# Kernel tuning notes

Measured on AMD Instinct MI355X. Metric: run time of the kernel, lower is better.

## Reference

```python
import jax, jax.numpy as jnp
import numpy as np

NUM_POINTS = 16384
OVERSAMPLE = 3
IMPORTANCE_RATIO = 0.75


def point_sample(feat, coords):
    """grid_sample(bilinear, align_corners=False, zero padding) at [0,1]^2 coords.
    feat: (N, C, H, W); coords: (N, P, 2) with coords[...,0]=x (width), [...,1]=y.
    Returns (N, C, P)."""
    N, C, H, W = feat.shape
    # grid_sample with g = 2c-1, align_corners=False -> pixel = c*size - 0.5
    x = coords[..., 0] * W - 0.5
    y = coords[..., 1] * H - 0.5
    x0 = jnp.floor(x)
    y0 = jnp.floor(y)
    x1 = x0 + 1.0
    y1 = y0 + 1.0
    wx1 = x - x0
    wx0 = 1.0 - wx1
    wy1 = y - y0
    wy0 = 1.0 - wy1
    featf = feat.reshape(N, C, H * W)

    def gather(yi, xi):
        valid = (xi >= 0) & (xi <= W - 1) & (yi >= 0) & (yi <= H - 1)
        xic = jnp.clip(xi, 0, W - 1).astype(jnp.int32)
        yic = jnp.clip(yi, 0, H - 1).astype(jnp.int32)
        idx = yic * W + xic  # (N, P)
        v = jnp.take_along_axis(featf, idx[:, None, :], axis=2)  # (N, C, P)
        return v * valid[:, None, :].astype(feat.dtype)

    out = (gather(y0, x0) * (wy0 * wx0)[:, None, :]
           + gather(y0, x1) * (wy0 * wx1)[:, None, :]
           + gather(y1, x0) * (wy1 * wx0)[:, None, :]
           + gather(y1, x1) * (wy1 * wx1)[:, None, :])
    return out


def calculate_uncertainty(logits):
    """logits: (N, C, P) -> (N, P) uncertainty = top2 - top1 (<= 0)."""
    if logits.shape[1] == 1:
        return -jnp.abs(logits)[:, 0, :]
    top2 = jax.lax.top_k(jnp.moveaxis(logits, 1, -1), 2)[0]  # (N, P, 2)
    return top2[..., 1] - top2[..., 0]


def sample_point_coords(coarse_logits):
    """get_uncertain_point_coords_with_randomness (torch.no_grad branch)."""
    N = coarse_logits.shape[0]
    num_sampled = NUM_POINTS * OVERSAMPLE
    num_imp = int(IMPORTANCE_RATIO * NUM_POINTS)
    num_rand = NUM_POINTS - num_imp
    k1, k2 = jax.random.split(jax.random.key(7))
    cand = jax.random.uniform(k1, (N, num_sampled, 2), dtype=jnp.float32)
    cand_logits = point_sample(coarse_logits, cand)  # (N, C, S)
    unc = calculate_uncertainty(cand_logits)  # (N, S)
    idx = jax.lax.top_k(unc, num_imp)[1]  # (N, num_imp)
    imp = jnp.take_along_axis(cand, idx[..., None], axis=1)  # (N, num_imp, 2)
    rand = jax.random.uniform(k2, (N, num_rand, 2), dtype=jnp.float32)
    return jnp.concatenate([imp, rand], axis=1)  # (N, P, 2)


def point_head(fine, coarse_pts, w0, b0, w1, b1, w2, b2, wp, bp):
    x = jnp.concatenate([fine, coarse_pts], axis=1)  # (N, nin+C, P)
    for w, b in ((w0, b0), (w1, b1), (w2, b2)):
        x = jax.nn.relu(jnp.einsum('oc,ncp->nop', w, x) + b[None, :, None])
        x = jnp.concatenate([x, coarse_pts], axis=1)  # coarse_pred_each_layer
    return jnp.einsum('oc,ncp->nop', wp, x) + bp[None, :, None]  # (N, C, P)


def setup_inputs() -> dict:
    key = jax.random.key(0)
    ks = jax.random.split(key, 8)
    N, C, Hc, Wc = 8, 19, 64, 64
    nin, Hf, Wf = 256, 128, 128
    fin = nin + C  # 275
    return {
        'coarse_sem_seg_logits': jax.random.normal(ks[0], (N, C, Hc, Wc), jnp.float32),
        'features': jax.random.normal(ks[1], (N, nin, Hf, Wf), jnp.float32),
        'w0': jax.random.normal(ks[2], (nin, fin), jnp.float32) * (2.0 / fin) ** 0.5,
        'b0': jnp.zeros((nin,), jnp.float32),
        'w1': jax.random.normal(ks[3], (nin, fin), jnp.float32) * (2.0 / fin) ** 0.5,
        'b1': jnp.zeros((nin,), jnp.float32),
        'w2': jax.random.normal(ks[4], (nin, fin), jnp.float32) * (2.0 / fin) ** 0.5,
        'b2': jnp.zeros((nin,), jnp.float32),
        'wp': jax.random.normal(ks[5], (C, fin), jnp.float32) * 0.001,
        'bp': jnp.zeros((C,), jnp.float32),
    }


def reference(coarse_sem_seg_logits, features, w0, b0, w1, b1, w2, b2, wp, bp):
    # training-mode forward of PointRendSemSegHead
    point_coords = jax.lax.stop_gradient(
        sample_point_coords(jax.lax.stop_gradient(coarse_sem_seg_logits)))
    coarse_pts = point_sample(coarse_sem_seg_logits, point_coords)  # (N, C, P)
    fine_pts = point_sample(features, point_coords)  # (N, nin, P)
    point_logits = point_head(fine_pts, coarse_pts, w0, b0, w1, b1, w2, b2, wp, bp)
    return coarse_sem_seg_logits, point_logits, point_coords
```

## Files before the change

### kernel.cpp

```cpp
#include <hip/hip_runtime.h>
#include <stdint.h>

#pragma clang fp contract(off)

#define NB    8
#define CCH   19
#define CSTR  20
#define FCH   256
#define FIN   275
#define KP    288
#define NPTS  16384
#define NSAMP 49152
#define NIMP  12288
#define NRAND 4096
#define SORT_M 65536
#define CHUNK  8192
#define TP    64
#define XROW  608
#define WBF_OFF (4u << 20)
#define CTR_OFF (4718592u)
#define FTR_OFF (8u << 20)
#define FTR_BYTES (134217728ull / 2)

typedef __attribute__((ext_vector_type(8))) short bf16x8;
typedef __attribute__((ext_vector_type(4))) float f32x4;

__host__ __device__ __forceinline__ uint32_t rotl32(uint32_t v, int r) {
  return (v << r) | (v >> (32 - r));
}

__host__ __device__ __forceinline__ void tf2x32(uint32_t k0, uint32_t k1,
                                                uint32_t x0, uint32_t x1,
                                                uint32_t* o0, uint32_t* o1) {
  const uint32_t ks2 = k0 ^ k1 ^ 0x1BD11BDAu;
  x0 += k0; x1 += k1;
#define TF_R(r) { x0 += x1; x1 = rotl32(x1, (r)); x1 ^= x0; }
  TF_R(13) TF_R(15) TF_R(26) TF_R(6)
  x0 += k1;  x1 += ks2 + 1u;
  TF_R(17) TF_R(29) TF_R(16) TF_R(24)
  x0 += ks2; x1 += k0 + 2u;
  TF_R(13) TF_R(15) TF_R(26) TF_R(6)
  x0 += k0;  x1 += k1 + 3u;
  TF_R(17) TF_R(29) TF_R(16) TF_R(24)
  x0 += k1;  x1 += ks2 + 4u;
  TF_R(13) TF_R(15) TF_R(26) TF_R(6)
  x0 += ks2; x1 += k0 + 5u;
#undef TF_R
  *o0 = x0; *o1 = x1;
}

__device__ __forceinline__ float u01_at(uint32_t k0, uint32_t k1, uint32_t i) {
  uint32_t o0, o1;
  tf2x32(k0, k1, 0u, i, &o0, &o1);
  const uint32_t b = o0 ^ o1;
  const float f = __uint_as_float((b >> 9) | 0x3f800000u) - 1.0f;
  return fmaxf(0.0f, f);
}

__device__ __forceinline__ unsigned short f2bf(float f) {
  const uint32_t u = __float_as_uint(f);
  return (unsigned short)((u + 0x7fffu + ((u >> 16) & 1u)) >> 16);
}

__device__ __forceinline__ float bf2f(unsigned short h) {
  return __uint_as_float((uint32_t)h << 16);
}

template <int SZ>
__device__ __forceinline__ void interp(float cx, float cy, int* off, float* wgt) {
  const float X = cx * (float)SZ - 0.5f, Y = cy * (float)SZ - 0.5f;
  const float x0f = floorf(X), y0f = floorf(Y);
  const float fx = X - x0f, fy = Y - y0f;
  const float wx0 = 1.0f - fx, wy0 = 1.0f - fy;
  const int x0 = (int)x0f, y0 = (int)y0f;
  const int x0c = min(max(x0, 0), SZ - 1), x1c = min(max(x0 + 1, 0), SZ - 1);
  const int y0c = min(max(y0, 0), SZ - 1), y1c = min(max(y0 + 1, 0), SZ - 1);
  const bool vx0 = (x0 >= 0) & (x0 <= SZ - 1), vx1 = (x0 >= -1) & (x0 <= SZ - 2);
  const bool vy0 = (y0 >= 0) & (y0 <= SZ - 1), vy1 = (y0 >= -1) & (y0 <= SZ - 2);
  off[0] = y0c * SZ + x0c; wgt[0] = (vy0 & vx0) ? wy0 * wx0 : 0.0f;
  off[1] = y0c * SZ + x1c; wgt[1] = (vy0 & vx1) ? wy0 * fx  : 0.0f;
  off[2] = y1c * SZ + x0c; wgt[2] = (vy1 & vx0) ? fy  * wx0 : 0.0f;
  off[3] = y1c * SZ + x1c; wgt[3] = (vy1 & vx1) ? fy  * fx  : 0.0f;
}

__device__ __forceinline__ void ftr_tile_load(const float* __restrict__ feats,
                                              int ti, int tt,
                                              unsigned short (*tile)[66]) {
  const int nn = ti >> 10, ct = (ti >> 8) & 3, pt = ti & 255;
  const int c0 = ct * 64, p0 = pt * 64;
  const float* src = feats + ((size_t)nn << 22);
#pragma unroll 4
  for (int k = 0; k < 16; ++k) {
    const int c = 4 * k + (tt >> 6);
    const int p = tt & 63;
    tile[p][c] = f2bf(src[((size_t)(c0 + c) << 14) + p0 + p]);
  }
}

__device__ __forceinline__ void ftr_tile_store(unsigned short* __restrict__ ftr,
                                               int ti, int tt,
                                               unsigned short (*tile)[66]) {
  const int nn = ti >> 10, ct = (ti >> 8) & 3, pt = ti & 255;
  const int c0 = ct * 64, p0 = pt * 64;
  const int p = tt >> 2, q = tt & 3;
  const int cb = q * 16;
  uint32_t w[8];
#pragma unroll
  for (int m = 0; m < 8; ++m)
    w[m] = (uint32_t)tile[p][cb + 2 * m] | ((uint32_t)tile[p][cb + 2 * m + 1] << 16);
  unsigned short* dst = ftr + ((((size_t)nn << 14) + p0 + p) << 8) + c0 + cb;
  *(uint4*)(dst)     = make_uint4(w[0], w[1], w[2], w[3]);
  *(uint4*)(dst + 8) = make_uint4(w[4], w[5], w[6], w[7]);
}

__global__ __launch_bounds__(256) void prep(
    const float* __restrict__ coarse, float* __restrict__ ctr,
    const float* __restrict__ w0, const float* __restrict__ w1,
    const float* __restrict__ w2, const float* __restrict__ wpw,
    unsigned short* __restrict__ wbf, unsigned short* __restrict__ wpb) {
  __shared__ float tile[CCH][257];
  const int b = blockIdx.x, t = threadIdx.x;
  if (b < 128) {
    const int nn = b >> 4, px0 = (b & 15) * 256;
    const float* src = coarse + (size_t)nn * (CCH * 4096) + px0;
#pragma unroll
    for (int c = 0; c < CCH; ++c) tile[c][t] = src[c * 4096 + t];
    __syncthreads();
    float v[CSTR];
#pragma unroll
    for (int c = 0; c < CCH; ++c) v[c] = tile[c][t];
    v[19] = 0.0f;
    float* dst = ctr + ((size_t)(nn << 12) + px0 + t) * CSTR;
#pragma unroll
    for (int k = 0; k < 5; ++k) {
      f32x4 x; x[0] = v[4*k]; x[1] = v[4*k+1]; x[2] = v[4*k+2]; x[3] = v[4*k+3];
      *(f32x4*)(dst + 4 * k) = x;
    }
  } else {
    const int i = (b - 128) * 256 + t;
    if (i < 3 * 256 * KP) {
      const int L = i / (256 * KP);
      const int rem = i - L * (256 * KP);
      const int o = rem / KP, k = rem - o * KP;
      const float* W = (L == 0) ? w0 : (L == 1) ? w1 : w2;
      wbf[i] = (k < FIN) ? f2bf(W[o * FIN + k]) : (unsigned short)0;
    } else {
      const int j = i - 3 * 256 * KP;
      const int o = j / KP, k = j - o * KP;
      wpb[j] = (o < CCH && k < FIN) ? f2bf(wpw[o * FIN + k]) : (unsigned short)0;
    }
  }
}

__global__ __launch_bounds__(256) void unc_tr(
    const float* __restrict__ ctr, unsigned long long* __restrict__ keys,
    const float* __restrict__ feats, unsigned short* __restrict__ ftr,
    uint32_t k1a, uint32_t k1b, int tile0, int use_tr) {
  __shared__ unsigned short tile[64][66];
  const int bid = blockIdx.x, t = threadIdx.x;
  if (bid < 2048) {
    const int tid = bid * 256 + t;
    const int nn = tid >> 16, s = tid & (SORT_M - 1);
    if (s >= NSAMP) { keys[tid] = 0xFFFFFFFFFFFFFFFFull; return; }
    const uint32_t ci = (uint32_t)(((unsigned)nn * NSAMP + (unsigned)s) * 2);
    const float cx = u01_at(k1a, k1b, ci);
    const float cy = u01_at(k1a, k1b, ci + 1);
    const float X = cx * 64.0f - 0.5f, Y = cy * 64.0f - 0.5f;
    const float x0f = floorf(X), y0f = floorf(Y);
    const float fx = X - x0f, fy = Y - y0f;
    const float wx0 = 1.0f - fx, wy0 = 1.0f - fy;
    const int x0 = (int)x0f, y0 = (int)y0f;
    const int x0c = min(max(x0, 0), 63), x1c = min(max(x0 + 1, 0), 63);
    const int y0c = min(max(y0, 0), 63), y1c = min(max(y0 + 1, 0), 63);
    const bool vx0 = (x0 >= 0) & (x0 <= 63), vx1 = (x0 >= -1) & (x0 <= 62);
    const bool vy0 = (y0 >= 0) & (y0 <= 63), vy1 = (y0 >= -1) & (y0 <= 62);
    const float w00 = (vy0 & vx0) ? wy0 * wx0 : 0.0f;
    const float w01 = (vy0 & vx1) ? wy0 * fx  : 0.0f;
    const float w10 = (vy1 & vx0) ? fy  * wx0 : 0.0f;
    const float w11 = (vy1 & vx1) ? fy  * fx  : 0.0f;
    const float* rb = ctr + ((size_t)nn << 12) * CSTR;
    const float* r0 = rb + (size_t)(y0c * 64 + x0c) * CSTR;
    const float* r1 = rb + (size_t)(y0c * 64 + x1c) * CSTR;
    const float* r2 = rb + (size_t)(y1c * 64 + x0c) * CSTR;
    const float* r3 = rb + (size_t)(y1c * 64 + x1c) * CSTR;
    float m1 = -3.402823466e38f, m2 = -3.402823466e38f;
#pragma unroll
    for (int k = 0; k < 5; ++k) {
      const f32x4 x0v = *(const f32x4*)(r0 + 4 * k);
      const f32x4 x1v = *(const f32x4*)(r1 + 4 * k);
      const f32x4 x2v = *(const f32x4*)(r2 + 4 * k);
      const f32x4 x3v = *(const f32x4*)(r3 + 4 * k);
#pragma unroll
      for (int e = 0; e < 4; ++e) {
        const int c = 4 * k + e;
        if (c < CCH) {
          const float v = ((x0v[e] * w00 + x1v[e] * w01) + x2v[e] * w10) + x3v[e] * w11;
          if (v > m1) { m2 = m1; m1 = v; } else if (v > m2) { m2 = v; }
        }
      }
    }
    const float unc = m2 - m1;
    const uint32_t b = __float_as_uint(unc);
    const uint32_t asc = (b & 0x80000000u) ? ~b : (b | 0x80000000u);
    keys[tid] = ((unsigned long long)(~asc) << 32) | (uint32_t)s;
  } else {
    if (!use_tr) return;
    const int ti = tile0 + (bid - 2048);
    ftr_tile_load(feats, ti, t, tile);
    __syncthreads();
    ftr_tile_store(ftr, ti, t, tile);
  }
}

__global__ __launch_bounds__(1024) void bitonic_local_tr(
    unsigned long long* __restrict__ keys,
    const float* __restrict__ feats, unsigned short* __restrict__ ftr,
    int tile0, int use_tr) {
  __shared__ unsigned long long s[CHUNK];
  const int b = blockIdx.x, t = threadIdx.x;
  if (b < 64) {
    unsigned long long* a = keys + (size_t)b * CHUNK;
    const unsigned gbase = (unsigned)(b * CHUNK) & (SORT_M - 1);
    for (int i = t; i < CHUNK; i += 1024) s[i] = a[i];
    __syncthreads();
    for (int k = 2; k <= CHUNK; k <<= 1) {
      for (int j = k >> 1; j > 0; j >>= 1) {
        for (int pid = t; pid < CHUNK / 2; pid += 1024) {
          const int i = ((pid & ~(j - 1)) << 1) | (pid & (j - 1));
          const int l = i | j;
          const bool up = (((gbase + i) & k) == 0);
          const unsigned long long x = s[i], y = s[l];
          if ((x > y) == up) { s[i] = y; s[l] = x; }
        }
        __syncthreads();
      }
    }
    for (int i = t; i < CHUNK; i += 1024) a[i] = s[i];
  } else {
    if (!use_tr) return;
    unsigned short (*tp)[66] =
        (unsigned short (*)[66])((char*)s + (size_t)(t >> 8) * (64 * 66 * 2));
    const int ti = tile0 + (b - 64) * 4 + (t >> 8);
    const int tt = t & 255;
    ftr_tile_load(feats, ti, tt, tp);
    __syncthreads();
    ftr_tile_store(ftr, ti, tt, tp);
  }
}

__global__ __launch_bounds__(256) void bitonic_global_tr(
    unsigned long long* __restrict__ keys, int k, int j, int ppb_shift, int nsort,
    const float* __restrict__ feats, unsigned short* __restrict__ ftr,
    int tile0, int use_tr) {
  __shared__ unsigned short tile[64][66];
  const int bb = blockIdx.x, tt = threadIdx.x;
  if (bb < nsort) {
    const int t = bb * 256 + tt;
    const int b = t >> ppb_shift, pid = t & ((1 << ppb_shift) - 1);
    const int i = ((pid & ~(j - 1)) << 1) | (pid & (j - 1));
    const int l = i | j;
    const bool up = ((i & k) == 0);
    unsigned long long* a = keys + ((size_t)b << 16);
    const unsigned long long x = a[i], y = a[l];
    if ((x > y) == up) { a[i] = y; a[l] = x; }
  } else {
    if (!use_tr) return;
    const int ti = tile0 + (bb - nsort);
    ftr_tile_load(feats, ti, tt, tile);
    __syncthreads();
    ftr_tile_store(ftr, ti, tt, tile);
  }
}

__global__ __launch_bounds__(1024) void bitonic_finish_tr(
    unsigned long long* __restrict__ keys, int k,
    const float* __restrict__ feats, unsigned short* __restrict__ ftr,
    int tile0, int use_tr) {
  __shared__ unsigned long long s[CHUNK];
  const int b = blockIdx.x, t = threadIdx.x;
  if (b < 64) {
    unsigned long long* a = keys + (size_t)b * CHUNK;
    const unsigned gi0 = (unsigned)(b * CHUNK) & (SORT_M - 1);
    for (int i = t; i < CHUNK; i += 1024) s[i] = a[i];
    __syncthreads();
    const bool up = ((gi0 & k) == 0);
    for (int j = CHUNK >> 1; j > 0; j >>= 1) {
      for (int pid = t; pid < CHUNK / 2; pid += 1024) {
        const int i = ((pid & ~(j - 1)) << 1) | (pid & (j - 1));
        const int l = i | j;
        const unsigned long long x = s[i], y = s[l];
        if ((x > y) == up) { s[i] = y; s[l] = x; }
      }
      __syncthreads();
    }
    for (int i = t; i < CHUNK; i += 1024) a[i] = s[i];
  } else {
    if (!use_tr) return;
    unsigned short (*tp)[66] =
        (unsigned short (*)[66])((char*)s + (size_t)(t >> 8) * (64 * 66 * 2));
    const int ti = tile0 + (b - 64) * 4 + (t >> 8);
    const int tt = t & 255;
    ftr_tile_load(feats, ti, tt, tp);
    __syncthreads();
    ftr_tile_store(ftr, ti, tt, tp);
  }
}

__global__ __launch_bounds__(1024) void finlow_tr(
    const unsigned long long* __restrict__ keys, float* __restrict__ outc,
    uint32_t k1a, uint32_t k1b, uint32_t k2a, uint32_t k2b,
    const float* __restrict__ feats, unsigned short* __restrict__ ftr,
    int tile0, int use_tr) {
  __shared__ unsigned long long s[CHUNK];
  const int b = blockIdx.x, t = threadIdx.x;
  if (b < 16) {
    const int nn = b >> 1, half = b & 1;
    const unsigned long long* a = keys + ((size_t)nn << 16) + half * CHUNK;
    for (int i = t; i < CHUNK; i += 1024) s[i] = a[i];
    __syncthreads();
    for (int j = CHUNK >> 1; j > 0; j >>= 1) {
      for (int pid = t; pid < CHUNK / 2; pid += 1024) {
        const int i = ((pid & ~(j - 1)) << 1) | (pid & (j - 1));
        const int l = i | j;
        const unsigned long long x = s[i], y = s[l];
        if (x > y) { s[i] = y; s[l] = x; }
      }
      __syncthreads();
    }
    const int pb = half * CHUNK;
    for (int q = t; q < CHUNK; q += 1024) {
      const int p = pb + q;
      float cx, cy;
      if (p < NIMP) {
        const unsigned idx = (unsigned)(s[q] & 0xFFFFFFFFu);
        const uint32_t ci = ((unsigned)nn * NSAMP + idx) * 2;
        cx = u01_at(k1a, k1b, ci);
        cy = u01_at(k1a, k1b, ci + 1);
      } else {
        const uint32_t ri = ((unsigned)nn * NRAND + (unsigned)(p - NIMP)) * 2;
        cx = u01_at(k2a, k2b, ri);
        cy = u01_at(k2a, k2b, ri + 1);
      }
      float* o = outc + (((size_t)nn << 14) + p) * 2;
      o[0] = cx; o[1] = cy;
    }
  } else {
    if (!use_tr) return;
    unsigned short (*tp)[66] =
        (unsigned short (*)[66])((char*)s + (size_t)(t >> 8) * (64 * 66 * 2));
    const int ti = tile0 + (b - 16) * 4 + (t >> 8);
    const int tt = t & 255;
    ftr_tile_load(feats, ti, tt, tp);
    __syncthreads();
    ftr_tile_store(ftr, ti, tt, tp);
  }
}

template <int USE_TR>
__global__ __launch_bounds__(512, 4) void fused_mfma(
    const float* __restrict__ coarse, const float* __restrict__ feats,
    const unsigned short* __restrict__ ftr, const float* __restrict__ ctr,
    const float* __restrict__ b0, const float* __restrict__ b1,
    const float* __restrict__ b2, const float* __restrict__ bp,
    const unsigned short* __restrict__ wbf, const unsigned short* __restrict__ wpb,
    const float* __restrict__ pc, float* __restrict__ outl) {
  __shared__ __align__(16) unsigned short xp[TP * (XROW / 2)];

  const int t = threadIdx.x;
  const int bid = ((int)blockIdx.x & 7) * 256 + ((int)blockIdx.x >> 3);
  const int nn = bid >> 8;
  const int pbase = (bid & 255) * TP;

  int offF[4]; float wgtF[4];
  int offC[4]; float wgtC[4];
  int offFc[4]; float wgtFc[4];
  {
    const float2 c = *(const float2*)(pc + ((size_t)nn * NPTS + pbase + (t >> 3)) * 2);
    interp<128>(c.x, c.y, offF, wgtF);
  }
  {
    const float2 c = *(const float2*)(pc + ((size_t)nn * NPTS + pbase + (t & 63)) * 2);
    interp<64>(c.x, c.y, offC, wgtC);
    if (!USE_TR) interp<128>(c.x, c.y, offFc, wgtFc);
  }

  if (USE_TR) {
    const int p = t >> 3, q = t & 7;
    const unsigned short* base = ftr + ((size_t)nn << 22) + q * 32;
    const unsigned short* n0 = base + ((size_t)offF[0] << 8);
    const unsigned short* n1 = base + ((size_t)offF[1] << 8);
    const unsigned short* n2 = base + ((size_t)offF[2] << 8);
    const unsigned short* n3 = base + ((size_t)offF[3] << 8);
    const float g0 = wgtF[0], g1 = wgtF[1], g2 = wgtF[2], g3 = wgtF[3];
    const unsigned swzp = (unsigned)(p & 7) << 4;
#pragma unroll
    for (int m = 0; m < 4; ++m) {
      const bf16x8 a = *(const bf16x8*)(n0 + m * 8);
      const bf16x8 bq = *(const bf16x8*)(n1 + m * 8);
      const bf16x8 c = *(const bf16x8*)(n2 + m * 8);
      const bf16x8 d = *(const bf16x8*)(n3 + m * 8);
      uint32_t u[4];
#pragma unroll
      for (int e = 0; e < 4; ++e) {
        float v0 = fmaf(bf2f((unsigned short)a[2 * e]), g0,
                   fmaf(bf2f((unsigned short)bq[2 * e]), g1,
                   fmaf(bf2f((unsigned short)c[2 * e]), g2,
                        bf2f((unsigned short)d[2 * e]) * g3)));
        float v1 = fmaf(bf2f((unsigned short)a[2 * e + 1]), g0,
                   fmaf(bf2f((unsigned short)bq[2 * e + 1]), g1,
                   fmaf(bf2f((unsigned short)c[2 * e + 1]), g2,
                        bf2f((unsigned short)d[2 * e + 1]) * g3)));
        u[e] = (uint32_t)f2bf(v0) | ((uint32_t)f2bf(v1) << 16);
      }
      *(uint4*)((char*)xp + p * XROW + (((unsigned)((q * 32 + m * 8) * 2)) ^ swzp)) =
          make_uint4(u[0], u[1], u[2], u[3]);
    }
    if (t < TP) {
      const int pp = t;
      const float* rb = ctr + ((size_t)nn << 12) * CSTR;
      const float* r0 = rb + (size_t)offC[0] * CSTR;
      const float* r1 = rb + (size_t)offC[1] * CSTR;
      const float* r2 = rb + (size_t)offC[2] * CSTR;
      const float* r3 = rb + (size_t)offC[3] * CSTR;
      const float h0 = wgtC[0], h1 = wgtC[1], h2 = wgtC[2], h3 = wgtC[3];
      unsigned short hs[32];
#pragma unroll
      for (int k = 0; k < 5; ++k) {
        const f32x4 x0v = *(const f32x4*)(r0 + 4 * k);
        const f32x4 x1v = *(const f32x4*)(r1 + 4 * k);
        const f32x4 x2v = *(const f32x4*)(r2 + 4 * k);
        const f32x4 x3v = *(const f32x4*)(r3 + 4 * k);
#pragma unroll
        for (int e = 0; e < 4; ++e) {
          const int c = 4 * k + e;
          if (c < CCH)
            hs[c] = f2bf(fmaf(x0v[e], h0, fmaf(x1v[e], h1,
                         fmaf(x2v[e], h2, x3v[e] * h3))));
        }
      }
#pragma unroll
      for (int c = CCH; c < 32; ++c) hs[c] = 0;
      const unsigned swzc = (unsigned)(pp & 7) << 4;
#pragma unroll
      for (int k = 0; k < 4; ++k) {
        uint4 u;
        u.x = (uint32_t)hs[8*k]   | ((uint32_t)hs[8*k+1] << 16);
        u.y = (uint32_t)hs[8*k+2] | ((uint32_t)hs[8*k+3] << 16);
        u.z = (uint32_t)hs[8*k+4] | ((uint32_t)hs[8*k+5] << 16);
        u.w = (uint32_t)hs[8*k+6] | ((uint32_t)hs[8*k+7] << 16);
        *(uint4*)((char*)xp + pp * XROW + (((unsigned)(512 + 16 * k)) ^ swzc)) = u;
      }
    }
  } else {
    for (int i = t; i < (KP / 2) * TP; i += 512) {
      const int p = i & (TP - 1);
      const int c0 = (i >> 6) * 2;
      float v0 = 0.0f, v1 = 0.0f;
      if (c0 < FCH) {
        const float* fb0 = feats + ((size_t)nn << 22) + ((size_t)c0 << 14);
        const float* fb1 = fb0 + 16384;
        v0 = ((fb0[offFc[0]] * wgtFc[0] + fb0[offFc[1]] * wgtFc[1])
             + fb0[offFc[2]] * wgtFc[2]) + fb0[offFc[3]] * wgtFc[3];
        v1 = ((fb1[offFc[0]] * wgtFc[0] + fb1[offFc[1]] * wgtFc[1])
             + fb1[offFc[2]] * wgtFc[2]) + fb1[offFc[3]] * wgtFc[3];
      } else if (c0 < FIN) {
        const float* cb0 = coarse + (size_t)nn * (CCH * 4096) + (size_t)(c0 - FCH) * 4096;
        v0 = ((cb0[offC[0]] * wgtC[0] + cb0[offC[1]] * wgtC[1])
             + cb0[offC[2]] * wgtC[2]) + cb0[offC[3]] * wgtC[3];
        if (c0 + 1 < FIN) {
          const float* cb1 = cb0 + 4096;
          v1 = ((cb1[offC[0]] * wgtC[0] + cb1[offC[1]] * wgtC[1])
               + cb1[offC[2]] * wgtC[2]) + cb1[offC[3]] * wgtC[3];
        }
      }
      const uint32_t u = (uint32_t)f2bf(v0) | ((uint32_t)f2bf(v1) << 16);
      *(uint32_t*)((char*)xp + p * XROW + (((unsigned)(c0 * 2)) ^ ((unsigned)(p & 7) << 4))) = u;
    }
  }

  const int lane = t & 63, wave = t >> 6;
  const int wm = wave & 3, wn = wave >> 2;
  const int l15 = lane & 15, g = lane >> 4;
  const unsigned swz = (unsigned)(l15 & 7) << 4;
  const char* xpB = (const char*)xp;

#pragma unroll
  for (int L = 0; L < 3; ++L) {
    __syncthreads();
    const float* Bv = (L == 0) ? b0 : (L == 1) ? b1 : b2;
    const unsigned short* wL = wbf + (size_t)L * (256 * KP);
    const unsigned short* wbase = wL + (size_t)(wm * 64 + l15) * KP + g * 8;

    f32x4 acc[4][2];
#pragma unroll
    for (int mt = 0; mt < 4; ++mt)
#pragma unroll
      for (int nt = 0; nt < 2; ++nt) acc[mt][nt] = (f32x4)(0.0f);

    bf16x8 a0 = *(const bf16x8*)(wbase + 0 * 16 * KP);
    bf16x8 a1 = *(const bf16x8*)(wbase + 1 * 16 * KP);
    bf16x8 a2 = *(const bf16x8*)(wbase + 2 * 16 * KP);
    bf16x8 a3 = *(const bf16x8*)(wbase + 3 * 16 * KP);
    for (int ks = 0; ks < 9; ++ks) {
      const bf16x8 c0v = a0, c1v = a1, c2v = a2, c3v = a3;
      if (ks < 8) {
        a0 = *(const bf16x8*)(wbase + 0 * 16 * KP + (ks + 1) * 32);
        a1 = *(const bf16x8*)(wbase + 1 * 16 * KP + (ks + 1) * 32);
        a2 = *(const bf16x8*)(wbase + 2 * 16 * KP + (ks + 1) * 32);
        a3 = *(const bf16x8*)(wbase + 3 * 16 * KP + (ks + 1) * 32);
      }
      const unsigned kb = (unsigned)(ks * 64 + g * 16) ^ swz;
      const bf16x8 q0 = *(const bf16x8*)(xpB + (wn * 32 + 0 + l15) * XROW + kb);
      const bf16x8 q1 = *(const bf16x8*)(xpB + (wn * 32 + 16 + l15) * XROW + kb);
      acc[0][0] = __builtin_amdgcn_mfma_f32_16x16x32_bf16(c0v, q0, acc[0][0], 0, 0, 0);
      acc[1][0] = __builtin_amdgcn_mfma_f32_16x16x32_bf16(c1v, q0, acc[1][0], 0, 0, 0);
      acc[2][0] = __builtin_amdgcn_mfma_f32_16x16x32_bf16(c2v, q0, acc[2][0], 0, 0, 0);
      acc[3][0] = __builtin_amdgcn_mfma_f32_16x16x32_bf16(c3v, q0, acc[3][0], 0, 0, 0);
      acc[0][1] = __builtin_amdgcn_mfma_f32_16x16x32_bf16(c0v, q1, acc[0][1], 0, 0, 0);
      acc[1][1] = __builtin_amdgcn_mfma_f32_16x16x32_bf16(c1v, q1, acc[1][1], 0, 0, 0);
      acc[2][1] = __builtin_amdgcn_mfma_f32_16x16x32_bf16(c2v, q1, acc[2][1], 0, 0, 0);
      acc[3][1] = __builtin_amdgcn_mfma_f32_16x16x32_bf16(c3v, q1, acc[3][1], 0, 0, 0);
    }
    __syncthreads();

#pragma unroll
    for (int mt = 0; mt < 4; ++mt) {
      const int ch0 = wm * 64 + mt * 16 + (g << 2);
      const float4 bv = *(const float4*)(Bv + ch0);
#pragma unroll
      for (int nt = 0; nt < 2; ++nt) {
        const int p = wn * 32 + nt * 16 + l15;
        const f32x4 v = acc[mt][nt];
        const unsigned short h0 = f2bf(fmaxf(v[0] + bv.x, 0.0f));
        const unsigned short h1 = f2bf(fmaxf(v[1] + bv.y, 0.0f));
        const unsigned short h2 = f2bf(fmaxf(v[2] + bv.z, 0.0f));
        const unsigned short h3 = f2bf(fmaxf(v[3] + bv.w, 0.0f));
        uint2 u;
        u.x = (uint32_t)h0 | ((uint32_t)h1 << 16);
        u.y = (uint32_t)h2 | ((uint32_t)h3 << 16);
        *(uint2*)((char*)xp + p * XROW + (((unsigned)(ch0 * 2)) ^ swz)) = u;
      }
    }
  }
  __syncthreads();

  const int hmt = wave >> 2, hnt = wave & 3;
  const unsigned short* hbase = wpb + (size_t)(hmt * 16 + l15) * KP + g * 8;
  f32x4 hacc = (f32x4)(0.0f);
  for (int ks = 0; ks < 9; ++ks) {
    const unsigned kb = (unsigned)(ks * 64 + g * 16) ^ swz;
    const bf16x8 ha = *(const bf16x8*)(hbase + ks * 32);
    const bf16x8 hb = *(const bf16x8*)(xpB + (hnt * 16 + l15) * XROW + kb);
    hacc = __builtin_amdgcn_mfma_f32_16x16x32_bf16(ha, hb, hacc, 0, 0, 0);
  }
  const int p = pbase + hnt * 16 + l15;
#pragma unroll
  for (int j = 0; j < 4; ++j) {
    const int ch = hmt * 16 + (g << 2) + j;
    if (ch < CCH)
      outl[((size_t)nn * CCH + ch) * NPTS + p] = hacc[j] + bp[ch];
  }
}

extern "C" void kernel_launch(void* const* d_in, const int* in_sizes, int n_in,
                              void* d_out, int out_size, void* d_ws, size_t ws_size,
                              hipStream_t stream) {
  const float* coarse = (const float*)d_in[0];
  const float* feats  = (const float*)d_in[1];
  const float* w0 = (const float*)d_in[2]; const float* b0 = (const float*)d_in[3];
  const float* w1 = (const float*)d_in[4]; const float* b1 = (const float*)d_in[5];
  const float* w2 = (const float*)d_in[6]; const float* b2 = (const float*)d_in[7];
  const float* wp = (const float*)d_in[8]; const float* bp = (const float*)d_in[9];

  float* out0 = (float*)d_out;
  float* outL = out0 + 622592;
  float* outC = outL + 2490368;

  unsigned long long* keys = (unsigned long long*)d_ws;
  unsigned short* wbf = (unsigned short*)((char*)d_ws + WBF_OFF);
  unsigned short* wpb = wbf + 3 * 256 * KP;
  float* ctr = (float*)((char*)d_ws + CTR_OFF);
  unsigned short* ftr = (unsigned short*)((char*)d_ws + FTR_OFF);
  const int use_tr = (ws_size >= (size_t)FTR_OFF + FTR_BYTES) ? 1 : 0;

  uint32_t k1a, k1b, k2a, k2b;
  tf2x32(0u, 7u, 0u, 0u, &k1a, &k1b);
  tf2x32(0u, 7u, 0u, 1u, &k2a, &k2b);

  hipMemcpyAsync(out0, coarse, 622592 * sizeof(float),
                 hipMemcpyDeviceToDevice, stream);

  prep<<<1028, 256, 0, stream>>>(coarse, ctr, w0, w1, w2, wp, wbf, wpb);

  const int NT = use_tr ? 1 : 0;
  unc_tr<<<2048 + NT * 1024, 256, 0, stream>>>(ctr, keys, feats, ftr,
                                               k1a, k1b, 0, use_tr);
  bitonic_local_tr<<<64 + NT * 192, 1024, 0, stream>>>(keys, feats, ftr, 1024, use_tr);
  bitonic_global_tr<<<1024 + NT * 896, 256, 0, stream>>>(keys, 16384, 8192, 15, 1024,
                                                         feats, ftr, 1792, use_tr);
  bitonic_finish_tr<<<64 + NT * 112, 1024, 0, stream>>>(keys, 16384, feats, ftr,
                                                        2688, use_tr);
  bitonic_global_tr<<<1024 + NT * 896, 256, 0, stream>>>(keys, 32768, 16384, 15, 1024,
                                                         feats, ftr, 3136, use_tr);
  bitonic_global_tr<<<1024 + NT * 896, 256, 0, stream>>>(keys, 32768, 8192, 15, 1024,
                                                         feats, ftr, 4032, use_tr);
  bitonic_finish_tr<<<64 + NT * 112, 1024, 0, stream>>>(keys, 32768, feats, ftr,
                                                        4928, use_tr);
  bitonic_global_tr<<<1024 + NT * 896, 256, 0, stream>>>(keys, 65536, 32768, 15, 1024,
                                                         feats, ftr, 5376, use_tr);
  bitonic_global_tr<<<512 + NT * 896, 256, 0, stream>>>(keys, 65536, 16384, 14, 512,
                                                        feats, ftr, 6272, use_tr);
  bitonic_global_tr<<<256 + NT * 896, 256, 0, stream>>>(keys, 65536, 8192, 13, 256,
                                                        feats, ftr, 7168, use_tr);
  finlow_tr<<<16 + NT * 32, 1024, 0, stream>>>(keys, outC, k1a, k1b, k2a, k2b,
                                               feats, ftr, 8064, use_tr);

  if (use_tr)
    fused_mfma<1><<<2048, 512, 0, stream>>>(coarse, feats, ftr, ctr, b0, b1, b2,
                                            bp, wbf, wpb, outC, outL);
  else
    fused_mfma<0><<<2048, 512, 0, stream>>>(coarse, feats, ftr, ctr, b0, b1, b2,
                                            bp, wbf, wpb, outC, outL);
}
```

Baseline: 361.2 us.

## Sort 16K-key chunks in LDS, drop global bitonic passes, fuse output copy

Doubles the shared-memory bitonic chunk to 16384 keys using 128KB of dynamic LDS. This removes three global bitonic merge passes and one finish kernel, and the final low-merge kernel now handles a whole batch per block. The D2D memcpy of the coarse logits is folded into the uncertainty kernel as extra float4-copy blocks, and XROW padding in the fused MFMA kernel changes from 608 to 640. The trade-off is far fewer sort-phase blocks (32 or 8) that may underfill the GPU, plus transpose tile indices that have to be redistributed across the launches.

```diff
diff --git a/kernel.cpp b/kernel.cpp
--- a/kernel.cpp
+++ b/kernel.cpp
@@ -14,13 +14,14 @@
 #define NIMP  12288
 #define NRAND 4096
 #define SORT_M 65536
-#define CHUNK  8192
+#define CHUNK2 16384
 #define TP    64
-#define XROW  608
+#define XROW  640
 #define WBF_OFF (4u << 20)
 #define CTR_OFF (4718592u)
 #define FTR_OFF (8u << 20)
 #define FTR_BYTES (134217728ull / 2)
+
 
 typedef __attribute__((ext_vector_type(8))) short bf16x8;
 typedef __attribute__((ext_vector_type(4))) float f32x4;
@@ -154,6 +155,7 @@
 
 __global__ __launch_bounds__(256) void unc_tr(
     const float* __restrict__ ctr, unsigned long long* __restrict__ keys,
+    const float* __restrict__ coarse, float* __restrict__ out0,
     const float* __restrict__ feats, unsigned short* __restrict__ ftr,
     uint32_t k1a, uint32_t k1b, int tile0, int use_tr) {
   __shared__ unsigned short tile[64][66];
@@ -203,44 +205,47 @@
     const uint32_t b = __float_as_uint(unc);
     const uint32_t asc = (b & 0x80000000u) ? ~b : (b | 0x80000000u);
     keys[tid] = ((unsigned long long)(~asc) << 32) | (uint32_t)s;
+  } else if (bid < 2656) {
+    const int i4 = (bid - 2048) * 256 + t;
+    ((float4*)out0)[i4] = ((const float4*)coarse)[i4];
   } else {
     if (!use_tr) return;
-    const int ti = tile0 + (bid - 2048);
+    const int ti = tile0 + (bid - 2656);
     ftr_tile_load(feats, ti, t, tile);
     __syncthreads();
     ftr_tile_store(ftr, ti, t, tile);
   }
 }
 
-__global__ __launch_bounds__(1024) void bitonic_local_tr(
+__global__ __launch_bounds__(1024) void bitonic_local2_tr(
     unsigned long long* __restrict__ keys,
     const float* __restrict__ feats, unsigned short* __restrict__ ftr,
     int tile0, int use_tr) {
-  __shared__ unsigned long long s[CHUNK];
+  extern __shared__ unsigned long long sA[];
   const int b = blockIdx.x, t = threadIdx.x;
-  if (b < 64) {
-    unsigned long long* a = keys + (size_t)b * CHUNK;
-    const unsigned gbase = (unsigned)(b * CHUNK) & (SORT_M - 1);
-    for (int i = t; i < CHUNK; i += 1024) s[i] = a[i];
-    __syncthreads();
-    for (int k = 2; k <= CHUNK; k <<= 1) {
+  if (b < 32) {
+    unsigned long long* a = keys + (size_t)b * CHUNK2;
+    const unsigned gbase = (unsigned)(b & 3) * CHUNK2;
+    for (int i = t; i < CHUNK2; i += 1024) sA[i] = a[i];
+    __syncthreads();
+    for (int k = 2; k <= CHUNK2; k <<= 1) {
       for (int j = k >> 1; j > 0; j >>= 1) {
-        for (int pid = t; pid < CHUNK / 2; pid += 1024) {
+        for (int pid = t; pid < CHUNK2 / 2; pid += 1024) {
           const int i = ((pid & ~(j - 1)) << 1) | (pid & (j - 1));
           const int l = i | j;
           const bool up = (((gbase + i) & k) == 0);
-          const unsigned long long x = s[i], y = s[l];
-          if ((x > y) == up) { s[i] = y; s[l] = x; }
+          const unsigned long long x = sA[i], y = sA[l];
+          if ((x > y) == up) { sA[i] = y; sA[l] = x; }
         }
         __syncthreads();
       }
     }
-    for (int i = t; i < CHUNK; i += 1024) a[i] = s[i];
+    for (int i = t; i < CHUNK2; i += 1024) a[i] = sA[i];
   } else {
     if (!use_tr) return;
     unsigned short (*tp)[66] =
-        (unsigned short (*)[66])((char*)s + (size_t)(t >> 8) * (64 * 66 * 2));
-    const int ti = tile0 + (b - 64) * 4 + (t >> 8);
+        (unsigned short (*)[66])((char*)sA + (size_t)(t >> 8) * (64 * 66 * 2));
+    const int ti = tile0 + (b - 32) * 4 + (t >> 8);
     const int tt = t & 255;
     ftr_tile_load(feats, ti, tt, tp);
     __syncthreads();
@@ -272,33 +277,33 @@
   }
 }
 
-__global__ __launch_bounds__(1024) void bitonic_finish_tr(
+__global__ __launch_bounds__(1024) void bitonic_finish2_tr(
     unsigned long long* __restrict__ keys, int k,
     const float* __restrict__ feats, unsigned short* __restrict__ ftr,
     int tile0, int use_tr) {
-  __shared__ unsigned long long s[CHUNK];
+  extern __shared__ unsigned long long sB[];
   const int b = blockIdx.x, t = threadIdx.x;
-  if (b < 64) {
-    unsigned long long* a = keys + (size_t)b * CHUNK;
-    const unsigned gi0 = (unsigned)(b * CHUNK) & (SORT_M - 1);
-    for (int i = t; i < CHUNK; i += 1024) s[i] = a[i];
-    __syncthreads();
-    const bool up = ((gi0 & k) == 0);
-    for (int j = CHUNK >> 1; j > 0; j >>= 1) {
-      for (int pid = t; pid < CHUNK / 2; pid += 1024) {
+  if (b < 32) {
+    unsigned long long* a = keys + (size_t)b * CHUNK2;
+    const unsigned gbase = (unsigned)((b & 3) * CHUNK2);
+    for (int i = t; i < CHUNK2; i += 1024) sB[i] = a[i];
+    __syncthreads();
+    const bool up = ((gbase & (unsigned)k) == 0);
+    for (int j = CHUNK2 >> 1; j > 0; j >>= 1) {
+      for (int pid = t; pid < CHUNK2 / 2; pid += 1024) {
         const int i = ((pid & ~(j - 1)) << 1) | (pid & (j - 1));
         const int l = i | j;
-        const unsigned long long x = s[i], y = s[l];
-        if ((x > y) == up) { s[i] = y; s[l] = x; }
+        const unsigned long long x = sB[i], y = sB[l];
+        if ((x > y) == up) { sB[i] = y; sB[l] = x; }
       }
       __syncthreads();
     }
-    for (int i = t; i < CHUNK; i += 1024) a[i] = s[i];
+    for (int i = t; i < CHUNK2; i += 1024) a[i] = sB[i];
   } else {
     if (!use_tr) return;
     unsigned short (*tp)[66] =
-        (unsigned short (*)[66])((char*)s + (size_t)(t >> 8) * (64 * 66 * 2));
-    const int ti = tile0 + (b - 64) * 4 + (t >> 8);
+        (unsigned short (*)[66])((char*)sB + (size_t)(t >> 8) * (64 * 66 * 2));
+    const int ti = tile0 + (b - 32) * 4 + (t >> 8);
     const int tt = t & 255;
     ftr_tile_load(feats, ti, tt, tp);
     __syncthreads();
@@ -306,49 +311,47 @@
   }
 }
 
-__global__ __launch_bounds__(1024) void finlow_tr(
+__global__ __launch_bounds__(1024) void finlow2_tr(
     const unsigned long long* __restrict__ keys, float* __restrict__ outc,
     uint32_t k1a, uint32_t k1b, uint32_t k2a, uint32_t k2b,
     const float* __restrict__ feats, unsigned short* __restrict__ ftr,
     int tile0, int use_tr) {
-  __shared__ unsigned long long s[CHUNK];
+  extern __shared__ unsigned long long sC[];
   const int b = blockIdx.x, t = threadIdx.x;
-  if (b < 16) {
-    const int nn = b >> 1, half = b & 1;
-    const unsigned long long* a = keys + ((size_t)nn << 16) + half * CHUNK;
-    for (int i = t; i < CHUNK; i += 1024) s[i] = a[i];
-    __syncthreads();
-    for (int j = CHUNK >> 1; j > 0; j >>= 1) {
-      for (int pid = t; pid < CHUNK / 2; pid += 1024) {
+  if (b < 8) {
+    const int nn = b;
+    const unsigned long long* a = keys + ((size_t)nn << 16);
+    for (int i = t; i < CHUNK2; i += 1024) sC[i] = a[i];
+    __syncthreads();
+    for (int j = CHUNK2 >> 1; j > 0; j >>= 1) {
+      for (int pid = t; pid < CHUNK2 / 2; pid += 1024) {
         const int i = ((pid & ~(j - 1)) << 1) | (pid & (j - 1));
         const int l = i | j;
-        const unsigned long long x = s[i], y = s[l];
-        if (x > y) { s[i] = y; s[l] = x; }
+        const unsigned long long x = sC[i], y = sC[l];
+        if (x > y) { sC[i] = y; sC[l] = x; }
       }
       __syncthreads();
     }
-    const int pb = half * CHUNK;
-    for (int q = t; q < CHUNK; q += 1024) {
-      const int p = pb + q;
+    for (int q = t; q < CHUNK2; q += 1024) {
       float cx, cy;
-      if (p < NIMP) {
-        const unsigned idx = (unsigned)(s[q] & 0xFFFFFFFFu);
+      if (q < NIMP) {
+        const unsigned idx = (unsigned)(sC[q] & 0xFFFFFFFFu);
         const uint32_t ci = ((unsigned)nn * NSAMP + idx) * 2;
         cx = u01_at(k1a, k1b, ci);
         cy = u01_at(k1a, k1b, ci + 1);
       } else {
-        const uint32_t ri = ((unsigned)nn * NRAND + (unsigned)(p - NIMP)) * 2;
+        const uint32_t ri = ((unsigned)nn * NRAND + (unsigned)(q - NIMP)) * 2;
         cx = u01_at(k2a, k2b, ri);
         cy = u01_at(k2a, k2b, ri + 1);
       }
-      float* o = outc + (((size_t)nn << 14) + p) * 2;
+      float* o = outc + (((size_t)nn << 14) + q) * 2;
       o[0] = cx; o[1] = cy;
     }
   } else {
     if (!use_tr) return;
     unsigned short (*tp)[66] =
-        (unsigned short (*)[66])((char*)s + (size_t)(t >> 8) * (64 * 66 * 2));
-    const int ti = tile0 + (b - 16) * 4 + (t >> 8);
+        (unsigned short (*)[66])((char*)sC + (size_t)(t >> 8) * (64 * 66 * 2));
+    const int ti = tile0 + (b - 8) * 4 + (t >> 8);
     const int tt = t & 255;
     ftr_tile_load(feats, ti, tt, tp);
     __syncthreads();
@@ -587,33 +590,23 @@
   tf2x32(0u, 7u, 0u, 0u, &k1a, &k1b);
   tf2x32(0u, 7u, 0u, 1u, &k2a, &k2b);
 
-  hipMemcpyAsync(out0, coarse, 622592 * sizeof(float),
-                 hipMemcpyDeviceToDevice, stream);
-
   prep<<<1028, 256, 0, stream>>>(coarse, ctr, w0, w1, w2, wp, wbf, wpb);
 
   const int NT = use_tr ? 1 : 0;
-  unc_tr<<<2048 + NT * 1024, 256, 0, stream>>>(ctr, keys, feats, ftr,
-                                               k1a, k1b, 0, use_tr);
-  bitonic_local_tr<<<64 + NT * 192, 1024, 0, stream>>>(keys, feats, ftr, 1024, use_tr);
-  bitonic_global_tr<<<1024 + NT * 896, 256, 0, stream>>>(keys, 16384, 8192, 15, 1024,
-                                                         feats, ftr, 1792, use_tr);
-  bitonic_finish_tr<<<64 + NT * 112, 1024, 0, stream>>>(keys, 16384, feats, ftr,
-                                                        2688, use_tr);
+  unc_tr<<<2656 + NT * 1024, 256, 0, stream>>>(ctr, keys, coarse, out0,
+                                               feats, ftr, k1a, k1b, 0, use_tr);
+  bitonic_local2_tr<<<32 + NT * 448, 1024, 131072, stream>>>(keys, feats, ftr,
+                                                             1024, use_tr);
   bitonic_global_tr<<<1024 + NT * 896, 256, 0, stream>>>(keys, 32768, 16384, 15, 1024,
-                                                         feats, ftr, 3136, use_tr);
-  bitonic_global_tr<<<1024 + NT * 896, 256, 0, stream>>>(keys, 32768, 8192, 15, 1024,
-                                                         feats, ftr, 4032, use_tr);
-  bitonic_finish_tr<<<64 + NT * 112, 1024, 0, stream>>>(keys, 32768, feats, ftr,
-                                                        4928, use_tr);
+                                                         feats, ftr, 2816, use_tr);
+  bitonic_finish2_tr<<<32 + NT * 448, 1024, 131072, stream>>>(keys, 32768, feats,
+                                                              ftr, 3712, use_tr);
   bitonic_global_tr<<<1024 + NT * 896, 256, 0, stream>>>(keys, 65536, 32768, 15, 1024,
-                                                         feats, ftr, 5376, use_tr);
+                                                         feats, ftr, 5504, use_tr);
   bitonic_global_tr<<<512 + NT * 896, 256, 0, stream>>>(keys, 65536, 16384, 14, 512,
-                                                        feats, ftr, 6272, use_tr);
-  bitonic_global_tr<<<256 + NT * 896, 256, 0, stream>>>(keys, 65536, 8192, 13, 256,
-                                                        feats, ftr, 7168, use_tr);
-  finlow_tr<<<16 + NT * 32, 1024, 0, stream>>>(keys, outC, k1a, k1b, k2a, k2b,
-                                               feats, ftr, 8064, use_tr);
+                                                        feats, ftr, 6400, use_tr);
+  finlow2_tr<<<8 + NT * 224, 1024, 131072, stream>>>(keys, outC, k1a, k1b, k2a, k2b,
+                                                     feats, ftr, 7296, use_tr);
 
   if (use_tr)
     fused_mfma<1><<<2048, 512, 0, stream>>>(coarse, feats, ftr, ctr, b0, b1, b2,
```

Measured after the change: 450.8 us. 24.8% more time.
